# Optimization experiments

Measured on AMD Instinct MI355X. Metric: run time of the kernel, lower is better.

The kernel has to match this reference:

```python
import jax, jax.numpy as jnp
import numpy as np

N_DR = 6_000_000
N_MR = 2_000_000
T = 20
# Izhikevich 'RS' parameters
A, B, C, D = 0.02, 0.2, -65.0, 8.0
V_SPIKE = 30.0
RATE_DECAY = 0.9  # rate EMA: r = 0.9*r + 0.1*spike


def setup_inputs() -> dict:
    key = jax.random.key(0)
    k1, k2 = jax.random.split(key)
    return {
        "noise_dr": jax.random.normal(k1, (T, N_DR), dtype=jnp.float32),
        "noise_mr": jax.random.normal(k2, (T, N_MR), dtype=jnp.float32),
        "v_dr": jnp.full((N_DR,), -65.0, dtype=jnp.float32),
        "u_dr": jnp.full((N_DR,), B * -65.0, dtype=jnp.float32),
        "rate_dr": jnp.zeros((N_DR,), dtype=jnp.float32),
        "v_mr": jnp.full((N_MR,), -65.0, dtype=jnp.float32),
        "u_mr": jnp.full((N_MR,), B * -65.0, dtype=jnp.float32),
        "rate_mr": jnp.zeros((N_MR,), dtype=jnp.float32),
    }


def _run_layer(v0, u0, r0, noise, i_base, i_tonic):
    """Run T Izhikevich steps over a neuron population via lax.scan."""
    def step(carry, n):
        v, u, r = carry
        I = i_base + i_tonic + 0.5 * n
        v = v + (0.04 * v * v + 5.0 * v + 140.0 - u + I)
        u = u + A * (B * v - u)
        spike = v >= V_SPIKE
        v = jnp.where(spike, C, v)
        u = jnp.where(spike, u + D, u)
        r = RATE_DECAY * r + (1.0 - RATE_DECAY) * spike.astype(v.dtype)
        return (v, u, r), None

    (v, u, r), _ = jax.lax.scan(step, (v0, u0, r0), noise)
    return v, u, r


def reference(noise_dr, noise_mr, v_dr, u_dr, rate_dr, v_mr, u_mr, rate_mr):
    # forward scalar defaults
    lhb_rate, ipn_raphe_drive, amygdala_stress, circadian = 0.0, 0.0, 0.0, 0.7
    base = 3.0 + circadian * 5.0 + ipn_raphe_drive * 12.0 - lhb_rate * 15.0 - amygdala_stress * 8.0
    # flee_active = False -> no -3.0
    i_dr = max(0.0, base)
    i_mr = max(0.0, base * 0.7)

    _, _, r_dr = _run_layer(v_dr, u_dr, rate_dr, noise_dr, i_dr, -0.5)
    _, _, r_mr = _run_layer(v_mr, u_mr, rate_mr, noise_mr, i_mr, -1.0)

    dr_mean = jnp.mean(r_dr)
    mr_mean = jnp.mean(r_mr)
    raw_ht5 = jnp.clip(dr_mean * 8.0, 0.0, 1.0)
    ema = 0.9 * 0.5 + 0.1 * raw_ht5  # _ht5_ema starts at 0.5
    ht5 = jnp.clip(ema, 0.05, 0.95)
    sensory_gain = 1.0 - 0.3 * ht5
    return jnp.stack([ht5, dr_mean, mr_mean, sensory_gain, ht5])
```

## Files before the change

kernel.cpp:

```cpp
#include <hip/hip_runtime.h>

#define P_A 0.02f
#define P_B 0.2f
#define P_C (-65.0f)
#define P_D 8.0f
#define V_SPIKE 30.0f

template <int T>
__global__ __launch_bounds__(256) void izh_layer_kernel(
    const float* __restrict__ noise,
    const float* __restrict__ v_in,
    const float* __restrict__ u_in,
    const float* __restrict__ r_in,
    float i_ext,
    long long N,
    float* __restrict__ accum)
{
    const long long tid  = (long long)blockIdx.x * blockDim.x + threadIdx.x;
    const long long base = tid * 4;

    float local = 0.0f;

    if (base + 3 < N) {
        float4 v4 = *(const float4*)(v_in + base);
        float4 u4 = *(const float4*)(u_in + base);
        float4 r4 = *(const float4*)(r_in + base);
        float v[4] = {v4.x, v4.y, v4.z, v4.w};
        float u[4] = {u4.x, u4.y, u4.z, u4.w};
        float r[4] = {r4.x, r4.y, r4.z, r4.w};

#pragma unroll
        for (int t = 0; t < T; ++t) {
            float4 n4 = *(const float4*)(noise + (long long)t * N + base);
            float n[4] = {n4.x, n4.y, n4.z, n4.w};
#pragma unroll
            for (int j = 0; j < 4; ++j) {
                float I  = i_ext + 0.5f * n[j];
                float vj = v[j];
                vj = vj + (0.04f * vj * vj + 5.0f * vj + 140.0f - u[j] + I);
                float uj = u[j] + P_A * (P_B * vj - u[j]);
                bool  s  = (vj >= V_SPIKE);
                v[j] = s ? P_C : vj;
                u[j] = s ? (uj + P_D) : uj;
                r[j] = 0.9f * r[j] + (s ? 0.1f : 0.0f);
            }
        }
        local = (r[0] + r[1]) + (r[2] + r[3]);
    } else if (base < N) {
        for (long long i = base; i < N; ++i) {
            float v = v_in[i], u = u_in[i], r = r_in[i];
            for (int t = 0; t < T; ++t) {
                float I = i_ext + 0.5f * noise[(long long)t * N + i];
                v = v + (0.04f * v * v + 5.0f * v + 140.0f - u + I);
                float uu = u + P_A * (P_B * v - u);
                bool s = (v >= V_SPIKE);
                v = s ? P_C : v;
                u = s ? (uu + P_D) : uu;
                r = 0.9f * r + (s ? 0.1f : 0.0f);
            }
            local += r;
        }
    }

#pragma unroll
    for (int off = 32; off > 0; off >>= 1)
        local += __shfl_down(local, off, 64);

    __shared__ float smem[4];
    const int lane = threadIdx.x & 63;
    const int wid  = threadIdx.x >> 6;
    if (lane == 0) smem[wid] = local;
    __syncthreads();
    if (threadIdx.x == 0) {
        float s = (smem[0] + smem[1]) + (smem[2] + smem[3]);
        atomicAdd(accum, s);
    }
}

__global__ void finalize_kernel(const float* __restrict__ accum,
                                float* __restrict__ out,
                                float inv_n_dr, float inv_n_mr)
{
    float dr_mean = accum[0] * inv_n_dr;
    float mr_mean = accum[1] * inv_n_mr;
    float raw  = fminf(fmaxf(dr_mean * 8.0f, 0.0f), 1.0f);
    float ema  = 0.9f * 0.5f + 0.1f * raw;
    float ht5  = fminf(fmaxf(ema, 0.05f), 0.95f);
    float gain = 1.0f - 0.3f * ht5;
    out[0] = ht5;
    out[1] = dr_mean;
    out[2] = mr_mean;
    out[3] = gain;
    out[4] = ht5;
}

extern "C" void kernel_launch(void* const* d_in, const int* in_sizes, int n_in,
                              void* d_out, int out_size, void* d_ws, size_t ws_size,
                              hipStream_t stream)
{
    const float* noise_dr = (const float*)d_in[0];
    const float* noise_mr = (const float*)d_in[1];
    const float* v_dr     = (const float*)d_in[2];
    const float* u_dr     = (const float*)d_in[3];
    const float* r_dr     = (const float*)d_in[4];
    const float* v_mr     = (const float*)d_in[5];
    const float* u_mr     = (const float*)d_in[6];
    const float* r_mr     = (const float*)d_in[7];
    float* out = (float*)d_out;

    const long long N_DR = 6000000LL;
    const long long N_MR = 2000000LL;
    constexpr int T = 20;

    const float i_ext_dr = fmaxf(0.0f, 3.0f + 0.7f * 5.0f) - 0.5f;
    const float i_ext_mr = fmaxf(0.0f, (3.0f + 0.7f * 5.0f) * 0.7f) - 1.0f;

    float* accum = (float*)d_ws;
    hipMemsetAsync(accum, 0, 2 * sizeof(float), stream);

    const int block = 256;
    const int grid_dr = (int)((N_DR / 4 + block - 1) / block);
    const int grid_mr = (int)((N_MR / 4 + block - 1) / block);

    izh_layer_kernel<T><<<grid_dr, block, 0, stream>>>(
        noise_dr, v_dr, u_dr, r_dr, i_ext_dr, N_DR, accum + 0);
    izh_layer_kernel<T><<<grid_mr, block, 0, stream>>>(
        noise_mr, v_mr, u_mr, r_mr, i_ext_mr, N_MR, accum + 1);

    finalize_kernel<<<1, 1, 0, stream>>>(accum, out,
                                         1.0f / (float)N_DR, 1.0f / (float)N_MR);
}
```

Before: 781.7 us.

## Fuse both neuron layers into one launch with deterministic partial-sum reduction

```diff
diff --git a/kernel.cpp b/kernel.cpp
--- a/kernel.cpp
+++ b/kernel.cpp
@@ -6,22 +6,36 @@
 #define P_D 8.0f
 #define V_SPIKE 30.0f
 
-template <int T>
-__global__ __launch_bounds__(256) void izh_layer_kernel(
-    const float* __restrict__ noise,
-    const float* __restrict__ v_in,
-    const float* __restrict__ u_in,
-    const float* __restrict__ r_in,
-    float i_ext,
-    long long N,
-    float* __restrict__ accum)
+#define T_STEPS 20
+#define BLOCK 256
+#define N_DR_I 6000000
+#define N_MR_I 2000000
+#define GRID_DR 5860
+#define GRID_MR 1954
+
+__global__ __launch_bounds__(BLOCK) void izh_fused_kernel(
+    const float* __restrict__ noise_dr,
+    const float* __restrict__ noise_mr,
+    const float* __restrict__ v_dr, const float* __restrict__ u_dr, const float* __restrict__ r_dr,
+    const float* __restrict__ v_mr, const float* __restrict__ u_mr, const float* __restrict__ r_mr,
+    float i_ext_dr, float i_ext_mr,
+    float* __restrict__ ws_partial)
 {
-    const long long tid  = (long long)blockIdx.x * blockDim.x + threadIdx.x;
-    const long long base = tid * 4;
+    const bool is_dr = (blockIdx.x < GRID_DR);
+    const int  bid   = is_dr ? blockIdx.x : (blockIdx.x - GRID_DR);
+    const int  N     = is_dr ? N_DR_I : N_MR_I;
+    const float i_ext = is_dr ? i_ext_dr : i_ext_mr;
+    const float* __restrict__ noise = is_dr ? noise_dr : noise_mr;
+    const float* __restrict__ v_in  = is_dr ? v_dr : v_mr;
+    const float* __restrict__ u_in  = is_dr ? u_dr : u_mr;
+    const float* __restrict__ r_in  = is_dr ? r_dr : r_mr;
+
+    const int tid  = bid * BLOCK + (int)threadIdx.x;
+    const int base = tid * 4;
 
     float local = 0.0f;
 
-    if (base + 3 < N) {
+    if (base < N) {
         float4 v4 = *(const float4*)(v_in + base);
         float4 u4 = *(const float4*)(u_in + base);
         float4 r4 = *(const float4*)(r_in + base);
@@ -29,9 +43,11 @@
         float u[4] = {u4.x, u4.y, u4.z, u4.w};
         float r[4] = {r4.x, r4.y, r4.z, r4.w};
 
+        const float* p = noise + base;
 #pragma unroll
-        for (int t = 0; t < T; ++t) {
-            float4 n4 = *(const float4*)(noise + (long long)t * N + base);
+        for (int t = 0; t < T_STEPS; ++t) {
+            float4 n4 = *(const float4*)p;
+            p += N;
             float n[4] = {n4.x, n4.y, n4.z, n4.w};
 #pragma unroll
             for (int j = 0; j < 4; ++j) {
@@ -46,20 +62,6 @@
             }
         }
         local = (r[0] + r[1]) + (r[2] + r[3]);
-    } else if (base < N) {
-        for (long long i = base; i < N; ++i) {
-            float v = v_in[i], u = u_in[i], r = r_in[i];
-            for (int t = 0; t < T; ++t) {
-                float I = i_ext + 0.5f * noise[(long long)t * N + i];
-                v = v + (0.04f * v * v + 5.0f * v + 140.0f - u + I);
-                float uu = u + P_A * (P_B * v - u);
-                bool s = (v >= V_SPIKE);
-                v = s ? P_C : v;
-                u = s ? (uu + P_D) : uu;
-                r = 0.9f * r + (s ? 0.1f : 0.0f);
-            }
-            local += r;
-        }
     }
 
 #pragma unroll
@@ -71,27 +73,41 @@
     const int wid  = threadIdx.x >> 6;
     if (lane == 0) smem[wid] = local;
     __syncthreads();
-    if (threadIdx.x == 0) {
-        float s = (smem[0] + smem[1]) + (smem[2] + smem[3]);
-        atomicAdd(accum, s);
-    }
+    if (threadIdx.x == 0)
+        ws_partial[blockIdx.x] = (smem[0] + smem[1]) + (smem[2] + smem[3]);
 }
 
-__global__ void finalize_kernel(const float* __restrict__ accum,
-                                float* __restrict__ out,
-                                float inv_n_dr, float inv_n_mr)
+__global__ __launch_bounds__(BLOCK) void finalize_kernel(
+    const float* __restrict__ ws_partial,
+    float* __restrict__ out)
 {
-    float dr_mean = accum[0] * inv_n_dr;
-    float mr_mean = accum[1] * inv_n_mr;
-    float raw  = fminf(fmaxf(dr_mean * 8.0f, 0.0f), 1.0f);
-    float ema  = 0.9f * 0.5f + 0.1f * raw;
-    float ht5  = fminf(fmaxf(ema, 0.05f), 0.95f);
-    float gain = 1.0f - 0.3f * ht5;
-    out[0] = ht5;
-    out[1] = dr_mean;
-    out[2] = mr_mean;
-    out[3] = gain;
-    out[4] = ht5;
+    float s_dr = 0.0f, s_mr = 0.0f;
+    for (int i = threadIdx.x; i < GRID_DR; i += BLOCK) s_dr += ws_partial[i];
+    for (int i = threadIdx.x; i < GRID_MR; i += BLOCK) s_mr += ws_partial[GRID_DR + i];
+
+#pragma unroll
+    for (int off = 32; off > 0; off >>= 1) {
+        s_dr += __shfl_down(s_dr, off, 64);
+        s_mr += __shfl_down(s_mr, off, 64);
+    }
+    __shared__ float smem_dr[4], smem_mr[4];
+    const int lane = threadIdx.x & 63;
+    const int wid  = threadIdx.x >> 6;
+    if (lane == 0) { smem_dr[wid] = s_dr; smem_mr[wid] = s_mr; }
+    __syncthreads();
+    if (threadIdx.x == 0) {
+        float dr_mean = ((smem_dr[0] + smem_dr[1]) + (smem_dr[2] + smem_dr[3])) * (1.0f / (float)N_DR_I);
+        float mr_mean = ((smem_mr[0] + smem_mr[1]) + (smem_mr[2] + smem_mr[3])) * (1.0f / (float)N_MR_I);
+        float raw  = fminf(fmaxf(dr_mean * 8.0f, 0.0f), 1.0f);
+        float ema  = 0.9f * 0.5f + 0.1f * raw;
+        float ht5  = fminf(fmaxf(ema, 0.05f), 0.95f);
+        float gain = 1.0f - 0.3f * ht5;
+        out[0] = ht5;
+        out[1] = dr_mean;
+        out[2] = mr_mean;
+        out[3] = gain;
+        out[4] = ht5;
+    }
 }
 
 extern "C" void kernel_launch(void* const* d_in, const int* in_sizes, int n_in,
@@ -108,25 +124,14 @@
     const float* r_mr     = (const float*)d_in[7];
     float* out = (float*)d_out;
 
-    const long long N_DR = 6000000LL;
-    const long long N_MR = 2000000LL;
-    constexpr int T = 20;
-
     const float i_ext_dr = fmaxf(0.0f, 3.0f + 0.7f * 5.0f) - 0.5f;
     const float i_ext_mr = fmaxf(0.0f, (3.0f + 0.7f * 5.0f) * 0.7f) - 1.0f;
 
-    float* accum = (float*)d_ws;
-    hipMemsetAsync(accum, 0, 2 * sizeof(float), stream);
+    float* ws_partial = (float*)d_ws;
 
-    const int block = 256;
-    const int grid_dr = (int)((N_DR / 4 + block - 1) / block);
-    const int grid_mr = (int)((N_MR / 4 + block - 1) / block);
+    izh_fused_kernel<<<GRID_DR + GRID_MR, BLOCK, 0, stream>>>(
+        noise_dr, noise_mr, v_dr, u_dr, r_dr, v_mr, u_mr, r_mr,
+        i_ext_dr, i_ext_mr, ws_partial);
 
-    izh_layer_kernel<T><<<grid_dr, block, 0, stream>>>(
-        noise_dr, v_dr, u_dr, r_dr, i_ext_dr, N_DR, accum + 0);
-    izh_layer_kernel<T><<<grid_mr, block, 0, stream>>>(
-        noise_mr, v_mr, u_mr, r_mr, i_ext_mr, N_MR, accum + 1);
-
-    finalize_kernel<<<1, 1, 0, stream>>>(accum, out,
-                                         1.0f / (float)N_DR, 1.0f / (float)N_MR);
+    finalize_kernel<<<1, BLOCK, 0, stream>>>(ws_partial, out);
 }
```

New measurement: 762.6 us. 1.03x faster.
